# Performance work log

Hardware: AMD Instinct MI355X
Metric: run time of the kernel (lower is better)

The kernel has to match this reference:

```python
import jax, jax.numpy as jnp
import numpy as np
import itertools

X_SAMPLES = 2
N_POINTS = 96
NUM_REPS = 4
DIMS = (1, 3, 5, 7)   # SO(3)-style rep dims 2l+1
MAX_DIM = 7
NUM_CG = 4            # CG multiplicity index 'g'
NUM_CH = 16
NUM_LAYERS = 3
L_INPUT = 3           # input rep index; DIMS[3] = 7 matches X's dim


def _cplx_contractor(n):
    # T[a1..an, k]: re/im components of i^(a1+...+an); contracting n (re,im)
    # pairs against T yields their complex product. Matches cplx_lib.cplx_contractor.
    comps = [(1.0, 0.0), (0.0, 1.0), (-1.0, 0.0), (0.0, -1.0)]
    T = np.zeros((2,) * (n + 1), dtype=np.float32)
    for idx in itertools.product((0, 1), repeat=n):
        re, im = comps[sum(idx) % 4]
        T[idx + (0,)] = re
        T[idx + (1,)] = im
    return T


def _make_cg(rng):
    # CG-like buffer with selection-rule sparsity: entries outside each rep's
    # true dimension are zero, and (l, m -> q) only couples when |l-m|<=q<=l+m.
    cg = rng.standard_normal((NUM_CG, NUM_REPS, MAX_DIM, NUM_REPS, MAX_DIM,
                              NUM_REPS, MAX_DIM, 2)).astype(np.float32)
    mask = np.zeros_like(cg)
    for l in range(NUM_REPS):
        for m in range(NUM_REPS):
            for q in range(NUM_REPS):
                if abs(l - m) <= q <= l + m:
                    mask[:, l, :DIMS[l], m, :DIMS[m], q, :DIMS[q], :] = 1.0
    return cg * mask


def setup_inputs() -> dict:
    key = jax.random.key(0)
    k1, k2, k3, k4 = jax.random.split(key, 4)
    X = jax.random.normal(k1, (X_SAMPLES, N_POINTS, DIMS[L_INPUT], 2), jnp.float32)
    V = jax.random.normal(k2, (X_SAMPLES, N_POINTS, NUM_REPS, NUM_CH, MAX_DIM, 2), jnp.float32)
    # per-layer parameters, init scales matching the torch module
    f = jax.random.normal(k3, (NUM_LAYERS, NUM_REPS, NUM_CG, 2), jnp.float32) / (NUM_REPS + 1) ** 2
    W = jax.random.normal(k4, (NUM_LAYERS, NUM_REPS, NUM_CH, NUM_CG, NUM_CH, 2), jnp.float32) / (NUM_CH + 1) ** 2
    cg = jnp.asarray(_make_cg(np.random.default_rng(0)))
    C4 = jnp.asarray(_cplx_contractor(4))
    return {"X": X, "l": L_INPUT, "V": V, "cg": cg, "f": f, "W": W, "C4": C4}


def reference(X, l, V, cg, f, W, C4):
    # dX[x,i,j] = X[x,j] - X[x,i]  (torch: -(X[:,:,None] - X[:,None,:]))
    dX = X[:, None, :, :, :] - X[:, :, None, :, :]
    x, n = X.shape[0], X.shape[1]
    num_reps, max_dim = cg.shape[1], cg.shape[2]
    dim_l = X.shape[-2]
    # filters: (x, n, n, num_reps, max_dim, 2) with dX embedded at rep l
    base = jnp.zeros((x, n, n, num_reps, max_dim, 2), X.dtype)
    base = base.at[:, :, :, l, :dim_l, :].set(dX)
    for k in range(f.shape[0]):
        # equivariant quadratic nonlinearity on the pairwise filters
        filt = base + jnp.einsum(
            'glsmtqrv,xijlsw,xijmty,qgz,vwyzk->xijqrk',
            cg, base, base, f[k], C4, optimize='optimal')
        # CG tensor-product of filters with features, mixing channels via W
        V = jnp.einsum(
            'glsmtqrv,xijlsw,xjmctu,qcgdy,vwuyz->xiqdrz',
            cg, filt, V, W[k], C4, optimize='optimal')
    return V
```

## Files before the change

### kernel.cpp

```cpp
#include <hip/hip_runtime.h>
#include <hip/hip_bf16.h>

#define XS   2
#define NP   96
#define NLAY 3
#define NXI  (XS*NP)
#define VBF_ARR (XS*256*96)

__constant__ int P2R_c[16] = {0, 1,1,1, 2,2,2,2,2, 3,3,3,3,3,3,3};
__constant__ int P2D_c[16] = {0, 0,1,2, 0,1,2,3,4, 0,1,2,3,4,5,6};
__constant__ int DIMS_c[4] = {1,3,5,7};
__constant__ int OFF_c[4]  = {0,1,4,9};

typedef __attribute__((ext_vector_type(8))) short bf16x8;
typedef __attribute__((ext_vector_type(4))) float f32x4;

__device__ inline float2 cmadd(float2 acc, float2 a, float2 b){
    acc.x += a.x*b.x - a.y*b.y;
    acc.y += a.x*b.y + a.y*b.x;
    return acc;
}
__device__ inline unsigned short f2bf(float v){
    __hip_bfloat16 h = __float2bfloat16(v);
    union { __hip_bfloat16 h; unsigned short u; } cv; cv.h = h; return cv.u;
}
__device__ inline float bf2f(unsigned short u){
    union { unsigned short u; __hip_bfloat16 h; } cv; cv.u = u;
    return __bfloat162float(cv.h);
}

__global__ __launch_bounds__(256)
void prep_filt_kernel(const float* __restrict__ cg,
                      const float* __restrict__ f,
                      const float* __restrict__ Vin,
                      const float* __restrict__ X,
                      unsigned short* __restrict__ PKbf,
                      unsigned short* __restrict__ Vbf0,
                      float* __restrict__ filt_g)
{
    __shared__ float2 cgf_s[784];
    __shared__ float2 dX_s[NP][7];

    const int tid = threadIdx.x;
    if (blockIdx.x < 256){
        int idx = blockIdx.x*256 + tid;
        if (idx < 16384){
            int id = idx;
            int lm = id & 255;
            int qg = id >> 8;
            int ls = lm >> 4, mt = lm & 15;
            int qr = qg >> 2, g = qg & 3;
            int l = P2R_c[ls], s = P2D_c[ls];
            int m = P2R_c[mt], t = P2D_c[mt];
            int q = P2R_c[qr], r = P2D_c[qr];
            size_t co = (((((((size_t)g*4 + l)*7 + s)*4 + m)*7 + t)*4 + q)*7 + r);
            float re = cg[co*2], im = cg[co*2+1];
            unsigned short rh = f2bf(re), rl = f2bf(re - bf2f(rh));
            unsigned short ih = f2bf(im), il = f2bf(im - bf2f(ih));
            PKbf[0*16384 + id] = rh;
            PKbf[1*16384 + id] = rl;
            PKbf[2*16384 + id] = ih;
            PKbf[3*16384 + id] = il;
            PKbf[4*16384 + id] = ih ^ 0x8000;
            PKbf[5*16384 + id] = il ^ 0x8000;
        } else {
            int id = idx - 16384;
            int kj = id % 96;
            int n  = (id / 96) % 256;
            int x  = id / (96*256);
            int mt = n >> 4, c = n & 15;
            int m = P2R_c[mt], t = P2D_c[mt];
            const float* p = Vin + ((((size_t)(x*NP + kj)*4 + m)*16 + c)*7 + t)*2;
            float re = p[0], im = p[1];
            unsigned short h;
            h = f2bf(re); Vbf0[0*VBF_ARR + id] = h;
            Vbf0[1*VBF_ARR + id] = f2bf(re - bf2f(h));
            h = f2bf(im); Vbf0[2*VBF_ARR + id] = h;
            Vbf0[3*VBF_ARR + id] = f2bf(im - bf2f(h));
        }
        return;
    }

    const int fb = blockIdx.x - 256;
    const int k  = fb / NXI;
    const int xi = fb % NXI;
    const int x = xi / NP, i = xi % NP;

    for (int u = tid; u < 784; u += 256){
        int qr = u / 49, st = u % 49;
        int s = st / 7, t = st % 7;
        int q = P2R_c[qr], r = P2D_c[qr];
        float2 acc = make_float2(0.f, 0.f);
        #pragma unroll
        for (int g = 0; g < 4; ++g){
            const float* cgp = cg + (((((((size_t)g*4+3)*7 + s)*4 + 3)*7 + t)*4 + q)*7 + r)*2;
            const float* fp  = f + ((k*4 + q)*4 + g)*2;
            acc = cmadd(acc, make_float2(cgp[0], cgp[1]), make_float2(fp[0], fp[1]));
        }
        cgf_s[u] = acc;
    }
    for (int e = tid; e < NP*7; e += 256){
        int j = e / 7, s = e % 7;
        const float* Xj = X + (((size_t)x*NP + j)*7 + s)*2;
        const float* Xi = X + (((size_t)x*NP + i)*7 + s)*2;
        dX_s[j][s] = make_float2(Xj[0]-Xi[0], Xj[1]-Xi[1]);
    }
    __syncthreads();

    float2* out = (float2*)filt_g + (size_t)fb*NP*16;
    for (int e = tid; e < NP*16; e += 256){
        int j = e >> 4, qr = e & 15;
        const float2* cb = cgf_s + qr*49;
        float2 acc = make_float2(0.f, 0.f);
        #pragma unroll
        for (int s = 0; s < 7; ++s){
            float2 inner = make_float2(0.f, 0.f);
            #pragma unroll
            for (int t = 0; t < 7; ++t)
                inner = cmadd(inner, cb[s*7 + t], dX_s[j][t]);
            acc = cmadd(acc, dX_s[j][s], inner);
        }
        if (qr >= 9){ float2 dv = dX_s[j][qr-9]; acc.x += dv.x; acc.y += dv.y; }
        out[e] = acc;
    }
}

template<int LAST>
__global__ __launch_bounds__(512, 2)
void TS_kernel(const float* __restrict__ filt_gk,
               const unsigned short* __restrict__ PKbf,
               const float* __restrict__ W_k,
               const unsigned short* __restrict__ Vbf_in,
               unsigned short* __restrict__ Vbf_out,
               float* __restrict__ Dout)
{
    __shared__ __align__(16) unsigned short Abuf[6][16][104];
    __shared__ __align__(16) unsigned short T2buf[4][16][264];
    float2* S_s = (float2*)&Abuf[0][0][0];

    const int tid = threadIdx.x;
    const int xi = blockIdx.x;
    const int x = xi / NP, i = xi % NP;

    for (int e = tid; e < NP*16; e += 512){
        const int j = e >> 4, ls = e & 15;
        float2 fv = ((const float2*)filt_gk)[((size_t)xi*NP + j)*16 + ls];
        unsigned short h = f2bf(fv.x);
        Abuf[0][ls][j] = h;
        Abuf[1][ls][j] = f2bf(fv.x - bf2f(h));
        h = f2bf(fv.y);
        unsigned short lo = f2bf(fv.y - bf2f(h));
        Abuf[2][ls][j] = h;
        Abuf[3][ls][j] = lo;
        Abuf[4][ls][j] = h  ^ 0x8000;
        Abuf[5][ls][j] = lo ^ 0x8000;
    }
    __syncthreads();

    const int w    = tid >> 6;
    const int lane = tid & 63;
    const int lrow = lane & 15;
    const int kb   = (lane >> 4) * 8;

    {
        f32x4 accR[2], accI[2];
        #pragma unroll
        for (int nt = 0; nt < 2; ++nt){
            accR[nt] = (f32x4){0.f,0.f,0.f,0.f};
            accI[nt] = (f32x4){0.f,0.f,0.f,0.f};
        }
        const unsigned short* Vrh = Vbf_in + 0*VBF_ARR + (size_t)x*256*96;
        const unsigned short* Vrl = Vbf_in + 1*VBF_ARR + (size_t)x*256*96;
        const unsigned short* Vih = Vbf_in + 2*VBF_ARR + (size_t)x*256*96;
        const unsigned short* Vil = Vbf_in + 3*VBF_ARR + (size_t)x*256*96;
        #pragma unroll
        for (int kt = 0; kt < 3; ++kt){
            const int ka = kt*32 + kb;
            bf16x8 frh = *(const bf16x8*)&Abuf[0][lrow][ka];
            bf16x8 frl = *(const bf16x8*)&Abuf[1][lrow][ka];
            bf16x8 fih = *(const bf16x8*)&Abuf[2][lrow][ka];
            bf16x8 fil = *(const bf16x8*)&Abuf[3][lrow][ka];
            bf16x8 nfh = *(const bf16x8*)&Abuf[4][lrow][ka];
            bf16x8 nfl = *(const bf16x8*)&Abuf[5][lrow][ka];
            #pragma unroll
            for (int nt = 0; nt < 2; ++nt){
                const int n = w*32 + nt*16 + lrow;
                const size_t bo = (size_t)n*96 + ka;
                bf16x8 vrh = *(const bf16x8*)(Vrh + bo);
                bf16x8 vrl = *(const bf16x8*)(Vrl + bo);
                bf16x8 vih = *(const bf16x8*)(Vih + bo);
                bf16x8 vil = *(const bf16x8*)(Vil + bo);
                accR[nt] = __builtin_amdgcn_mfma_f32_16x16x32_bf16(frh, vrh, accR[nt], 0,0,0);
                accR[nt] = __builtin_amdgcn_mfma_f32_16x16x32_bf16(frh, vrl, accR[nt], 0,0,0);
                accR[nt] = __builtin_amdgcn_mfma_f32_16x16x32_bf16(frl, vrh, accR[nt], 0,0,0);
                accR[nt] = __builtin_amdgcn_mfma_f32_16x16x32_bf16(nfh, vih, accR[nt], 0,0,0);
                accR[nt] = __builtin_amdgcn_mfma_f32_16x16x32_bf16(nfh, vil, accR[nt], 0,0,0);
                accR[nt] = __builtin_amdgcn_mfma_f32_16x16x32_bf16(nfl, vih, accR[nt], 0,0,0);
                accI[nt] = __builtin_amdgcn_mfma_f32_16x16x32_bf16(frh, vih, accI[nt], 0,0,0);
                accI[nt] = __builtin_amdgcn_mfma_f32_16x16x32_bf16(frh, vil, accI[nt], 0,0,0);
                accI[nt] = __builtin_amdgcn_mfma_f32_16x16x32_bf16(frl, vih, accI[nt], 0,0,0);
                accI[nt] = __builtin_amdgcn_mfma_f32_16x16x32_bf16(fih, vrh, accI[nt], 0,0,0);
                accI[nt] = __builtin_amdgcn_mfma_f32_16x16x32_bf16(fih, vrl, accI[nt], 0,0,0);
                accI[nt] = __builtin_amdgcn_mfma_f32_16x16x32_bf16(fil, vrh, accI[nt], 0,0,0);
            }
        }
        #pragma unroll
        for (int nt = 0; nt < 2; ++nt){
            #pragma unroll
            for (int r = 0; r < 4; ++r){
                const int lmp = ((lane>>4)*4 + r)*16 + (w*2 + nt);
                float tr = accR[nt][r], ti = accI[nt][r];
                unsigned short h = f2bf(tr);
                T2buf[0][lrow][lmp] = h;
                T2buf[1][lrow][lmp] = f2bf(tr - bf2f(h));
                h = f2bf(ti);
                T2buf[2][lrow][lmp] = h;
                T2buf[3][lrow][lmp] = f2bf(ti - bf2f(h));
            }
        }
    }
    __syncthreads();

    {
        const int qtile = w & 3;
        const int kh    = w >> 2;
        f32x4 sR = (f32x4){0.f,0.f,0.f,0.f};
        f32x4 sI = (f32x4){0.f,0.f,0.f,0.f};
        #pragma unroll
        for (int kt4 = 0; kt4 < 4; ++kt4){
            const int kt = kh*4 + kt4;
            const int ka = kt*32 + kb;
            const size_t arow = (size_t)(qtile*16 + lrow)*256 + ka;
            bf16x8 prh = *(const bf16x8*)(PKbf + 0*16384 + arow);
            bf16x8 prl = *(const bf16x8*)(PKbf + 1*16384 + arow);
            bf16x8 pih = *(const bf16x8*)(PKbf + 2*16384 + arow);
            bf16x8 pil = *(const bf16x8*)(PKbf + 3*16384 + arow);
            bf16x8 pnh = *(const bf16x8*)(PKbf + 4*16384 + arow);
            bf16x8 pnl = *(const bf16x8*)(PKbf + 5*16384 + arow);
            bf16x8 trh = *(const bf16x8*)&T2buf[0][lrow][ka];
            bf16x8 trl = *(const bf16x8*)&T2buf[1][lrow][ka];
            bf16x8 tih = *(const bf16x8*)&T2buf[2][lrow][ka];
            bf16x8 til = *(const bf16x8*)&T2buf[3][lrow][ka];
            sR = __builtin_amdgcn_mfma_f32_16x16x32_bf16(prh, trh, sR, 0,0,0);
            sR = __builtin_amdgcn_mfma_f32_16x16x32_bf16(prh, trl, sR, 0,0,0);
            sR = __builtin_amdgcn_mfma_f32_16x16x32_bf16(prl, trh, sR, 0,0,0);
            sR = __builtin_amdgcn_mfma_f32_16x16x32_bf16(pnh, tih, sR, 0,0,0);
            sR = __builtin_amdgcn_mfma_f32_16x16x32_bf16(pnh, til, sR, 0,0,0);
            sR = __builtin_amdgcn_mfma_f32_16x16x32_bf16(pnl, tih, sR, 0,0,0);
            sI = __builtin_amdgcn_mfma_f32_16x16x32_bf16(prh, tih, sI, 0,0,0);
            sI = __builtin_amdgcn_mfma_f32_16x16x32_bf16(prh, til, sI, 0,0,0);
            sI = __builtin_amdgcn_mfma_f32_16x16x32_bf16(prl, tih, sI, 0,0,0);
            sI = __builtin_amdgcn_mfma_f32_16x16x32_bf16(pih, trh, sI, 0,0,0);
            sI = __builtin_amdgcn_mfma_f32_16x16x32_bf16(pih, trl, sI, 0,0,0);
            sI = __builtin_amdgcn_mfma_f32_16x16x32_bf16(pil, trh, sI, 0,0,0);
        }
        if (kh == 0){
            #pragma unroll
            for (int r = 0; r < 4; ++r)
                S_s[((size_t)qtile*16 + (lane>>4)*4 + r)*16 + lrow] =
                    make_float2(sR[r], sI[r]);
        }
        __syncthreads();
        if (kh == 1){
            #pragma unroll
            for (int r = 0; r < 4; ++r){
                const size_t si = ((size_t)qtile*16 + (lane>>4)*4 + r)*16 + lrow;
                float2 sp = S_s[si];
                sp.x += sR[r]; sp.y += sI[r];
                S_s[si] = sp;
            }
        }
        __syncthreads();
    }

    if (tid < 256){
        const int qr2 = tid >> 4, d = tid & 15;
        const int q = P2R_c[qr2];
        float2 acc = make_float2(0.f, 0.f);
        const float2* Wb = (const float2*)W_k + (size_t)q*16*4*16 + d;
        #pragma unroll 4
        for (int c = 0; c < 16; ++c){
            #pragma unroll
            for (int g = 0; g < 4; ++g){
                acc = cmadd(acc, S_s[((size_t)qr2*4 + g)*16 + c], Wb[(c*4 + g)*16]);
            }
        }
        if (LAST){
            const int r = P2D_c[qr2];
            ((float2*)Dout)[((size_t)xi*4 + q)*112 + d*7 + r] = acc;
        } else {
            const size_t vo = ((size_t)x*256 + tid)*96 + i;
            unsigned short h;
            h = f2bf(acc.x); Vbf_out[0*VBF_ARR + vo] = h;
            Vbf_out[1*VBF_ARR + vo] = f2bf(acc.x - bf2f(h));
            h = f2bf(acc.y); Vbf_out[2*VBF_ARR + vo] = h;
            Vbf_out[3*VBF_ARR + vo] = f2bf(acc.y - bf2f(h));
        }
    } else if (LAST){
        const int u = tid - 256;
        if (u < 192){
            int q, base, span;
            if (u < 96)      { q = 0; base = 0;   span = 6; }
            else if (u < 160){ q = 1; base = 96;  span = 4; }
            else             { q = 2; base = 160; span = 2; }
            const int v = u - base;
            const int d = v / span;
            const int r = DIMS_c[q] + v % span;
            ((float2*)Dout)[((size_t)xi*4 + q)*112 + d*7 + r] = make_float2(0.f, 0.f);
        }
    }
}

extern "C" void kernel_launch(void* const* d_in, const int* in_sizes, int n_in,
                              void* d_out, int out_size, void* d_ws, size_t ws_size,
                              hipStream_t stream) {
    const float* X  = (const float*)d_in[0];
    const float* V  = (const float*)d_in[2];
    const float* cg = (const float*)d_in[3];
    const float* f  = (const float*)d_in[4];
    const float* W  = (const float*)d_in[5];

    float* ws    = (float*)d_ws;
    unsigned short* PKbf = (unsigned short*)ws;
    unsigned short* VbfA = (unsigned short*)(ws + 49152);
    unsigned short* VbfB = (unsigned short*)(ws + 49152 + 98304);
    float* filt_g = ws + 49152 + 98304 + 98304;

    prep_filt_kernel<<<256 + NLAY*NXI, 256, 0, stream>>>(cg, f, V, X, PKbf, VbfA, filt_g);

    const float* W0 = W;
    const float* W1 = W + (size_t)1*4*16*4*16*2;
    const float* W2 = W + (size_t)2*4*16*4*16*2;
    const float* f0 = filt_g;
    const float* f1 = filt_g + (size_t)1*NXI*NP*16*2;
    const float* f2 = filt_g + (size_t)2*NXI*NP*16*2;

    TS_kernel<0><<<NXI, 512, 0, stream>>>(f0, PKbf, W0, VbfA, VbfB, nullptr);
    TS_kernel<0><<<NXI, 512, 0, stream>>>(f1, PKbf, W1, VbfB, VbfA, nullptr);
    TS_kernel<1><<<NXI, 512, 0, stream>>>(f2, PKbf, W2, VbfA, VbfB, (float*)d_out);
}
```

Baseline: 69.27 us.

## Fuse prep and three layer kernels into one cooperative kernel with grid syncs

Replaces the four separate launches (prep/filter plus three tensor-product layers) with a single cooperative kernel of 192 blocks that uses grid-wide syncs between layers. Each block now computes its own per-layer filter directly into shared memory as split bf16, instead of writing fp32 filters to global memory and reading them back. This removes launch gaps and the global filter round trip. In exchange it adds grid barrier costs, runs the initial packing on fewer threads, and depends on all blocks being co-resident.

```diff
diff --git a/kernel.cpp b/kernel.cpp
--- a/kernel.cpp
+++ b/kernel.cpp
@@ -1,5 +1,6 @@
 #include <hip/hip_runtime.h>
 #include <hip/hip_bf16.h>
+#include <hip/hip_cooperative_groups.h>
 
 #define XS   2
 #define NP   96
@@ -7,6 +8,8 @@
 #define NXI  (XS*NP)
 #define VBF_ARR (XS*256*96)
 
+namespace cgx = cooperative_groups;
+
 __constant__ int P2R_c[16] = {0, 1,1,1, 2,2,2,2,2, 3,3,3,3,3,3,3};
 __constant__ int P2D_c[16] = {0, 0,1,2, 0,1,2,3,4, 0,1,2,3,4,5,6};
 __constant__ int DIMS_c[4] = {1,3,5,7};
@@ -29,23 +32,33 @@
     return __bfloat162float(cv.h);
 }
 
-__global__ __launch_bounds__(256)
-void prep_filt_kernel(const float* __restrict__ cg,
-                      const float* __restrict__ f,
-                      const float* __restrict__ Vin,
-                      const float* __restrict__ X,
-                      unsigned short* __restrict__ PKbf,
-                      unsigned short* __restrict__ Vbf0,
-                      float* __restrict__ filt_g)
+__global__ __launch_bounds__(512)
+void fused_kernel(const float* __restrict__ cg,
+                  const float* __restrict__ f,
+                  const float* __restrict__ Vin,
+                  const float* __restrict__ X,
+                  const float* __restrict__ W,
+                  unsigned short* __restrict__ PKbf,
+                  unsigned short* __restrict__ VbfA,
+                  unsigned short* __restrict__ VbfB,
+                  float* __restrict__ Dout)
 {
+    __shared__ float2 dX_s[NP][7];
     __shared__ float2 cgf_s[784];
-    __shared__ float2 dX_s[NP][7];
+    __shared__ __align__(16) unsigned short Abuf[6][16][104];
+    __shared__ __align__(16) unsigned short T2buf[4][16][264];
+    float2* S_s = (float2*)&Abuf[0][0][0];
+
+    cgx::grid_group grid = cgx::this_grid();
 
     const int tid = threadIdx.x;
-    if (blockIdx.x < 256){
-        int idx = blockIdx.x*256 + tid;
-        if (idx < 16384){
-            int id = idx;
+    const int xi = blockIdx.x;
+    const int x = xi / NP, i = xi % NP;
+
+    {
+        const int gidx = xi*512 + tid;
+        if (gidx < 16384){
+            int id = gidx;
             int lm = id & 255;
             int qg = id >> 8;
             int ls = lm >> 4, mt = lm & 15;
@@ -63,250 +76,232 @@
             PKbf[3*16384 + id] = il;
             PKbf[4*16384 + id] = ih ^ 0x8000;
             PKbf[5*16384 + id] = il ^ 0x8000;
-        } else {
-            int id = idx - 16384;
+        } else if (gidx < 65536){
+            int id = gidx - 16384;
             int kj = id % 96;
             int n  = (id / 96) % 256;
-            int x  = id / (96*256);
+            int xx = id / (96*256);
             int mt = n >> 4, c = n & 15;
             int m = P2R_c[mt], t = P2D_c[mt];
-            const float* p = Vin + ((((size_t)(x*NP + kj)*4 + m)*16 + c)*7 + t)*2;
+            const float* p = Vin + ((((size_t)(xx*NP + kj)*4 + m)*16 + c)*7 + t)*2;
             float re = p[0], im = p[1];
             unsigned short h;
-            h = f2bf(re); Vbf0[0*VBF_ARR + id] = h;
-            Vbf0[1*VBF_ARR + id] = f2bf(re - bf2f(h));
-            h = f2bf(im); Vbf0[2*VBF_ARR + id] = h;
-            Vbf0[3*VBF_ARR + id] = f2bf(im - bf2f(h));
-        }
-        return;
+            h = f2bf(re); VbfA[0*VBF_ARR + id] = h;
+            VbfA[1*VBF_ARR + id] = f2bf(re - bf2f(h));
+            h = f2bf(im); VbfA[2*VBF_ARR + id] = h;
+            VbfA[3*VBF_ARR + id] = f2bf(im - bf2f(h));
+        }
     }
-
-    const int fb = blockIdx.x - 256;
-    const int k  = fb / NXI;
-    const int xi = fb % NXI;
-    const int x = xi / NP, i = xi % NP;
-
-    for (int u = tid; u < 784; u += 256){
-        int qr = u / 49, st = u % 49;
-        int s = st / 7, t = st % 7;
-        int q = P2R_c[qr], r = P2D_c[qr];
-        float2 acc = make_float2(0.f, 0.f);
-        #pragma unroll
-        for (int g = 0; g < 4; ++g){
-            const float* cgp = cg + (((((((size_t)g*4+3)*7 + s)*4 + 3)*7 + t)*4 + q)*7 + r)*2;
-            const float* fp  = f + ((k*4 + q)*4 + g)*2;
-            acc = cmadd(acc, make_float2(cgp[0], cgp[1]), make_float2(fp[0], fp[1]));
-        }
-        cgf_s[u] = acc;
-    }
-    for (int e = tid; e < NP*7; e += 256){
+    for (int e = tid; e < NP*7; e += 512){
         int j = e / 7, s = e % 7;
         const float* Xj = X + (((size_t)x*NP + j)*7 + s)*2;
         const float* Xi = X + (((size_t)x*NP + i)*7 + s)*2;
         dX_s[j][s] = make_float2(Xj[0]-Xi[0], Xj[1]-Xi[1]);
     }
-    __syncthreads();
-
-    float2* out = (float2*)filt_g + (size_t)fb*NP*16;
-    for (int e = tid; e < NP*16; e += 256){
-        int j = e >> 4, qr = e & 15;
-        const float2* cb = cgf_s + qr*49;
-        float2 acc = make_float2(0.f, 0.f);
-        #pragma unroll
-        for (int s = 0; s < 7; ++s){
-            float2 inner = make_float2(0.f, 0.f);
-            #pragma unroll
-            for (int t = 0; t < 7; ++t)
-                inner = cmadd(inner, cb[s*7 + t], dX_s[j][t]);
-            acc = cmadd(acc, dX_s[j][s], inner);
-        }
-        if (qr >= 9){ float2 dv = dX_s[j][qr-9]; acc.x += dv.x; acc.y += dv.y; }
-        out[e] = acc;
-    }
-}
-
-template<int LAST>
-__global__ __launch_bounds__(512, 2)
-void TS_kernel(const float* __restrict__ filt_gk,
-               const unsigned short* __restrict__ PKbf,
-               const float* __restrict__ W_k,
-               const unsigned short* __restrict__ Vbf_in,
-               unsigned short* __restrict__ Vbf_out,
-               float* __restrict__ Dout)
-{
-    __shared__ __align__(16) unsigned short Abuf[6][16][104];
-    __shared__ __align__(16) unsigned short T2buf[4][16][264];
-    float2* S_s = (float2*)&Abuf[0][0][0];
-
-    const int tid = threadIdx.x;
-    const int xi = blockIdx.x;
-    const int x = xi / NP, i = xi % NP;
-
-    for (int e = tid; e < NP*16; e += 512){
-        const int j = e >> 4, ls = e & 15;
-        float2 fv = ((const float2*)filt_gk)[((size_t)xi*NP + j)*16 + ls];
-        unsigned short h = f2bf(fv.x);
-        Abuf[0][ls][j] = h;
-        Abuf[1][ls][j] = f2bf(fv.x - bf2f(h));
-        h = f2bf(fv.y);
-        unsigned short lo = f2bf(fv.y - bf2f(h));
-        Abuf[2][ls][j] = h;
-        Abuf[3][ls][j] = lo;
-        Abuf[4][ls][j] = h  ^ 0x8000;
-        Abuf[5][ls][j] = lo ^ 0x8000;
-    }
-    __syncthreads();
+    __threadfence();
+    grid.sync();
 
     const int w    = tid >> 6;
     const int lane = tid & 63;
     const int lrow = lane & 15;
     const int kb   = (lane >> 4) * 8;
 
-    {
-        f32x4 accR[2], accI[2];
-        #pragma unroll
-        for (int nt = 0; nt < 2; ++nt){
-            accR[nt] = (f32x4){0.f,0.f,0.f,0.f};
-            accI[nt] = (f32x4){0.f,0.f,0.f,0.f};
-        }
-        const unsigned short* Vrh = Vbf_in + 0*VBF_ARR + (size_t)x*256*96;
-        const unsigned short* Vrl = Vbf_in + 1*VBF_ARR + (size_t)x*256*96;
-        const unsigned short* Vih = Vbf_in + 2*VBF_ARR + (size_t)x*256*96;
-        const unsigned short* Vil = Vbf_in + 3*VBF_ARR + (size_t)x*256*96;
-        #pragma unroll
-        for (int kt = 0; kt < 3; ++kt){
-            const int ka = kt*32 + kb;
-            bf16x8 frh = *(const bf16x8*)&Abuf[0][lrow][ka];
-            bf16x8 frl = *(const bf16x8*)&Abuf[1][lrow][ka];
-            bf16x8 fih = *(const bf16x8*)&Abuf[2][lrow][ka];
-            bf16x8 fil = *(const bf16x8*)&Abuf[3][lrow][ka];
-            bf16x8 nfh = *(const bf16x8*)&Abuf[4][lrow][ka];
-            bf16x8 nfl = *(const bf16x8*)&Abuf[5][lrow][ka];
+    for (int k = 0; k < NLAY; ++k){
+        const unsigned short* Vbf_in  = (k & 1) ? VbfB : VbfA;
+        unsigned short*       Vbf_out = (k & 1) ? VbfA : VbfB;
+        const float* W_k = W + (size_t)k*4*16*4*16*2;
+
+        for (int u = tid; u < 784; u += 512){
+            int qr = u / 49, st = u % 49;
+            int s = st / 7, t = st % 7;
+            int q = P2R_c[qr], r = P2D_c[qr];
+            float2 acc = make_float2(0.f, 0.f);
+            #pragma unroll
+            for (int g = 0; g < 4; ++g){
+                const float* cgp = cg + (((((((size_t)g*4+3)*7 + s)*4 + 3)*7 + t)*4 + q)*7 + r)*2;
+                const float* fp  = f + ((k*4 + q)*4 + g)*2;
+                acc = cmadd(acc, make_float2(cgp[0], cgp[1]), make_float2(fp[0], fp[1]));
+            }
+            cgf_s[u] = acc;
+        }
+        __syncthreads();
+
+        for (int e = tid; e < NP*16; e += 512){
+            int j = e >> 4, qr = e & 15;
+            const float2* cb = cgf_s + qr*49;
+            float2 acc = make_float2(0.f, 0.f);
+            #pragma unroll
+            for (int s = 0; s < 7; ++s){
+                float2 inner = make_float2(0.f, 0.f);
+                #pragma unroll
+                for (int t = 0; t < 7; ++t)
+                    inner = cmadd(inner, cb[s*7 + t], dX_s[j][t]);
+                acc = cmadd(acc, dX_s[j][s], inner);
+            }
+            if (qr >= 9){ float2 dv = dX_s[j][qr-9]; acc.x += dv.x; acc.y += dv.y; }
+            unsigned short h = f2bf(acc.x);
+            Abuf[0][qr][j] = h;
+            Abuf[1][qr][j] = f2bf(acc.x - bf2f(h));
+            h = f2bf(acc.y);
+            unsigned short lo = f2bf(acc.y - bf2f(h));
+            Abuf[2][qr][j] = h;
+            Abuf[3][qr][j] = lo;
+            Abuf[4][qr][j] = h  ^ 0x8000;
+            Abuf[5][qr][j] = lo ^ 0x8000;
+        }
+        __syncthreads();
+
+        {
+            f32x4 accR[2], accI[2];
             #pragma unroll
             for (int nt = 0; nt < 2; ++nt){
-                const int n = w*32 + nt*16 + lrow;
-                const size_t bo = (size_t)n*96 + ka;
-                bf16x8 vrh = *(const bf16x8*)(Vrh + bo);
-                bf16x8 vrl = *(const bf16x8*)(Vrl + bo);
-                bf16x8 vih = *(const bf16x8*)(Vih + bo);
-                bf16x8 vil = *(const bf16x8*)(Vil + bo);
-                accR[nt] = __builtin_amdgcn_mfma_f32_16x16x32_bf16(frh, vrh, accR[nt], 0,0,0);
-                accR[nt] = __builtin_amdgcn_mfma_f32_16x16x32_bf16(frh, vrl, accR[nt], 0,0,0);
-                accR[nt] = __builtin_amdgcn_mfma_f32_16x16x32_bf16(frl, vrh, accR[nt], 0,0,0);
-                accR[nt] = __builtin_amdgcn_mfma_f32_16x16x32_bf16(nfh, vih, accR[nt], 0,0,0);
-                accR[nt] = __builtin_amdgcn_mfma_f32_16x16x32_bf16(nfh, vil, accR[nt], 0,0,0);
-                accR[nt] = __builtin_amdgcn_mfma_f32_16x16x32_bf16(nfl, vih, accR[nt], 0,0,0);
-                accI[nt] = __builtin_amdgcn_mfma_f32_16x16x32_bf16(frh, vih, accI[nt], 0,0,0);
-                accI[nt] = __builtin_amdgcn_mfma_f32_16x16x32_bf16(frh, vil, accI[nt], 0,0,0);
-                accI[nt] = __builtin_amdgcn_mfma_f32_16x16x32_bf16(frl, vih, accI[nt], 0,0,0);
-                accI[nt] = __builtin_amdgcn_mfma_f32_16x16x32_bf16(fih, vrh, accI[nt], 0,0,0);
-                accI[nt] = __builtin_amdgcn_mfma_f32_16x16x32_bf16(fih, vrl, accI[nt], 0,0,0);
-                accI[nt] = __builtin_amdgcn_mfma_f32_16x16x32_bf16(fil, vrh, accI[nt], 0,0,0);
-            }
-        }
-        #pragma unroll
-        for (int nt = 0; nt < 2; ++nt){
-            #pragma unroll
-            for (int r = 0; r < 4; ++r){
-                const int lmp = ((lane>>4)*4 + r)*16 + (w*2 + nt);
-                float tr = accR[nt][r], ti = accI[nt][r];
-                unsigned short h = f2bf(tr);
-                T2buf[0][lrow][lmp] = h;
-                T2buf[1][lrow][lmp] = f2bf(tr - bf2f(h));
-                h = f2bf(ti);
-                T2buf[2][lrow][lmp] = h;
-                T2buf[3][lrow][lmp] = f2bf(ti - bf2f(h));
-            }
-        }
-    }
-    __syncthreads();
-
-    {
-        const int qtile = w & 3;
-        const int kh    = w >> 2;
-        f32x4 sR = (f32x4){0.f,0.f,0.f,0.f};
-        f32x4 sI = (f32x4){0.f,0.f,0.f,0.f};
-        #pragma unroll
-        for (int kt4 = 0; kt4 < 4; ++kt4){
-            const int kt = kh*4 + kt4;
-            const int ka = kt*32 + kb;
-            const size_t arow = (size_t)(qtile*16 + lrow)*256 + ka;
-            bf16x8 prh = *(const bf16x8*)(PKbf + 0*16384 + arow);
-            bf16x8 prl = *(const bf16x8*)(PKbf + 1*16384 + arow);
-            bf16x8 pih = *(const bf16x8*)(PKbf + 2*16384 + arow);
-            bf16x8 pil = *(const bf16x8*)(PKbf + 3*16384 + arow);
-            bf16x8 pnh = *(const bf16x8*)(PKbf + 4*16384 + arow);
-            bf16x8 pnl = *(const bf16x8*)(PKbf + 5*16384 + arow);
-            bf16x8 trh = *(const bf16x8*)&T2buf[0][lrow][ka];
-            bf16x8 trl = *(const bf16x8*)&T2buf[1][lrow][ka];
-            bf16x8 tih = *(const bf16x8*)&T2buf[2][lrow][ka];
-            bf16x8 til = *(const bf16x8*)&T2buf[3][lrow][ka];
-            sR = __builtin_amdgcn_mfma_f32_16x16x32_bf16(prh, trh, sR, 0,0,0);
-            sR = __builtin_amdgcn_mfma_f32_16x16x32_bf16(prh, trl, sR, 0,0,0);
-            sR = __builtin_amdgcn_mfma_f32_16x16x32_bf16(prl, trh, sR, 0,0,0);
-            sR = __builtin_amdgcn_mfma_f32_16x16x32_bf16(pnh, tih, sR, 0,0,0);
-            sR = __builtin_amdgcn_mfma_f32_16x16x32_bf16(pnh, til, sR, 0,0,0);
-            sR = __builtin_amdgcn_mfma_f32_16x16x32_bf16(pnl, tih, sR, 0,0,0);
-            sI = __builtin_amdgcn_mfma_f32_16x16x32_bf16(prh, tih, sI, 0,0,0);
-            sI = __builtin_amdgcn_mfma_f32_16x16x32_bf16(prh, til, sI, 0,0,0);
-            sI = __builtin_amdgcn_mfma_f32_16x16x32_bf16(prl, tih, sI, 0,0,0);
-            sI = __builtin_amdgcn_mfma_f32_16x16x32_bf16(pih, trh, sI, 0,0,0);
-            sI = __builtin_amdgcn_mfma_f32_16x16x32_bf16(pih, trl, sI, 0,0,0);
-            sI = __builtin_amdgcn_mfma_f32_16x16x32_bf16(pil, trh, sI, 0,0,0);
-        }
-        if (kh == 0){
-            #pragma unroll
-            for (int r = 0; r < 4; ++r)
-                S_s[((size_t)qtile*16 + (lane>>4)*4 + r)*16 + lrow] =
-                    make_float2(sR[r], sI[r]);
+                accR[nt] = (f32x4){0.f,0.f,0.f,0.f};
+                accI[nt] = (f32x4){0.f,0.f,0.f,0.f};
+            }
+            const unsigned short* Vrh = Vbf_in + 0*VBF_ARR + (size_t)x*256*96;
+            const unsigned short* Vrl = Vbf_in + 1*VBF_ARR + (size_t)x*256*96;
+            const unsigned short* Vih = Vbf_in + 2*VBF_ARR + (size_t)x*256*96;
+            const unsigned short* Vil = Vbf_in + 3*VBF_ARR + (size_t)x*256*96;
+            #pragma unroll
+            for (int kt = 0; kt < 3; ++kt){
+                const int ka = kt*32 + kb;
+                bf16x8 frh = *(const bf16x8*)&Abuf[0][lrow][ka];
+                bf16x8 frl = *(const bf16x8*)&Abuf[1][lrow][ka];
+                bf16x8 fih = *(const bf16x8*)&Abuf[2][lrow][ka];
+                bf16x8 fil = *(const bf16x8*)&Abuf[3][lrow][ka];
+                bf16x8 nfh = *(const bf16x8*)&Abuf[4][lrow][ka];
+                bf16x8 nfl = *(const bf16x8*)&Abuf[5][lrow][ka];
+                #pragma unroll
+                for (int nt = 0; nt < 2; ++nt){
+                    const int n = w*32 + nt*16 + lrow;
+                    const size_t bo = (size_t)n*96 + ka;
+                    bf16x8 vrh = *(const bf16x8*)(Vrh + bo);
+                    bf16x8 vrl = *(const bf16x8*)(Vrl + bo);
+                    bf16x8 vih = *(const bf16x8*)(Vih + bo);
+                    bf16x8 vil = *(const bf16x8*)(Vil + bo);
+                    accR[nt] = __builtin_amdgcn_mfma_f32_16x16x32_bf16(frh, vrh, accR[nt], 0,0,0);
+                    accR[nt] = __builtin_amdgcn_mfma_f32_16x16x32_bf16(frh, vrl, accR[nt], 0,0,0);
+                    accR[nt] = __builtin_amdgcn_mfma_f32_16x16x32_bf16(frl, vrh, accR[nt], 0,0,0);
+                    accR[nt] = __builtin_amdgcn_mfma_f32_16x16x32_bf16(nfh, vih, accR[nt], 0,0,0);
+                    accR[nt] = __builtin_amdgcn_mfma_f32_16x16x32_bf16(nfh, vil, accR[nt], 0,0,0);
+                    accR[nt] = __builtin_amdgcn_mfma_f32_16x16x32_bf16(nfl, vih, accR[nt], 0,0,0);
+                    accI[nt] = __builtin_amdgcn_mfma_f32_16x16x32_bf16(frh, vih, accI[nt], 0,0,0);
+                    accI[nt] = __builtin_amdgcn_mfma_f32_16x16x32_bf16(frh, vil, accI[nt], 0,0,0);
+                    accI[nt] = __builtin_amdgcn_mfma_f32_16x16x32_bf16(frl, vih, accI[nt], 0,0,0);
+                    accI[nt] = __builtin_amdgcn_mfma_f32_16x16x32_bf16(fih, vrh, accI[nt], 0,0,0);
+                    accI[nt] = __builtin_amdgcn_mfma_f32_16x16x32_bf16(fih, vrl, accI[nt], 0,0,0);
+                    accI[nt] = __builtin_amdgcn_mfma_f32_16x16x32_bf16(fil, vrh, accI[nt], 0,0,0);
+                }
+            }
+            #pragma unroll
+            for (int nt = 0; nt < 2; ++nt){
+                #pragma unroll
+                for (int r = 0; r < 4; ++r){
+                    const int lmp = ((lane>>4)*4 + r)*16 + (w*2 + nt);
+                    float tr = accR[nt][r], ti = accI[nt][r];
+                    unsigned short h = f2bf(tr);
+                    T2buf[0][lrow][lmp] = h;
+                    T2buf[1][lrow][lmp] = f2bf(tr - bf2f(h));
+                    h = f2bf(ti);
+                    T2buf[2][lrow][lmp] = h;
+                    T2buf[3][lrow][lmp] = f2bf(ti - bf2f(h));
+                }
+            }
         }
         __syncthreads();
-        if (kh == 1){
-            #pragma unroll
-            for (int r = 0; r < 4; ++r){
-                const size_t si = ((size_t)qtile*16 + (lane>>4)*4 + r)*16 + lrow;
-                float2 sp = S_s[si];
-                sp.x += sR[r]; sp.y += sI[r];
-                S_s[si] = sp;
-            }
-        }
-        __syncthreads();
-    }
-
-    if (tid < 256){
-        const int qr2 = tid >> 4, d = tid & 15;
-        const int q = P2R_c[qr2];
-        float2 acc = make_float2(0.f, 0.f);
-        const float2* Wb = (const float2*)W_k + (size_t)q*16*4*16 + d;
-        #pragma unroll 4
-        for (int c = 0; c < 16; ++c){
-            #pragma unroll
-            for (int g = 0; g < 4; ++g){
-                acc = cmadd(acc, S_s[((size_t)qr2*4 + g)*16 + c], Wb[(c*4 + g)*16]);
-            }
-        }
-        if (LAST){
-            const int r = P2D_c[qr2];
-            ((float2*)Dout)[((size_t)xi*4 + q)*112 + d*7 + r] = acc;
-        } else {
-            const size_t vo = ((size_t)x*256 + tid)*96 + i;
-            unsigned short h;
-            h = f2bf(acc.x); Vbf_out[0*VBF_ARR + vo] = h;
-            Vbf_out[1*VBF_ARR + vo] = f2bf(acc.x - bf2f(h));
-            h = f2bf(acc.y); Vbf_out[2*VBF_ARR + vo] = h;
-            Vbf_out[3*VBF_ARR + vo] = f2bf(acc.y - bf2f(h));
-        }
-    } else if (LAST){
-        const int u = tid - 256;
-        if (u < 192){
-            int q, base, span;
-            if (u < 96)      { q = 0; base = 0;   span = 6; }
-            else if (u < 160){ q = 1; base = 96;  span = 4; }
-            else             { q = 2; base = 160; span = 2; }
-            const int v = u - base;
-            const int d = v / span;
-            const int r = DIMS_c[q] + v % span;
-            ((float2*)Dout)[((size_t)xi*4 + q)*112 + d*7 + r] = make_float2(0.f, 0.f);
+
+        {
+            const int qtile = w & 3;
+            const int kh    = w >> 2;
+            f32x4 sR = (f32x4){0.f,0.f,0.f,0.f};
+            f32x4 sI = (f32x4){0.f,0.f,0.f,0.f};
+            #pragma unroll
+            for (int kt4 = 0; kt4 < 4; ++kt4){
+                const int kt = kh*4 + kt4;
+                const int ka = kt*32 + kb;
+                const size_t arow = (size_t)(qtile*16 + lrow)*256 + ka;
+                bf16x8 prh = *(const bf16x8*)(PKbf + 0*16384 + arow);
+                bf16x8 prl = *(const bf16x8*)(PKbf + 1*16384 + arow);
+                bf16x8 pih = *(const bf16x8*)(PKbf + 2*16384 + arow);
+                bf16x8 pil = *(const bf16x8*)(PKbf + 3*16384 + arow);
+                bf16x8 pnh = *(const bf16x8*)(PKbf + 4*16384 + arow);
+                bf16x8 pnl = *(const bf16x8*)(PKbf + 5*16384 + arow);
+                bf16x8 trh = *(const bf16x8*)&T2buf[0][lrow][ka];
+                bf16x8 trl = *(const bf16x8*)&T2buf[1][lrow][ka];
+                bf16x8 tih = *(const bf16x8*)&T2buf[2][lrow][ka];
+                bf16x8 til = *(const bf16x8*)&T2buf[3][lrow][ka];
+                sR = __builtin_amdgcn_mfma_f32_16x16x32_bf16(prh, trh, sR, 0,0,0);
+                sR = __builtin_amdgcn_mfma_f32_16x16x32_bf16(prh, trl, sR, 0,0,0);
+                sR = __builtin_amdgcn_mfma_f32_16x16x32_bf16(prl, trh, sR, 0,0,0);
+                sR = __builtin_amdgcn_mfma_f32_16x16x32_bf16(pnh, tih, sR, 0,0,0);
+                sR = __builtin_amdgcn_mfma_f32_16x16x32_bf16(pnh, til, sR, 0,0,0);
+                sR = __builtin_amdgcn_mfma_f32_16x16x32_bf16(pnl, tih, sR, 0,0,0);
+                sI = __builtin_amdgcn_mfma_f32_16x16x32_bf16(prh, tih, sI, 0,0,0);
+                sI = __builtin_amdgcn_mfma_f32_16x16x32_bf16(prh, til, sI, 0,0,0);
+                sI = __builtin_amdgcn_mfma_f32_16x16x32_bf16(prl, tih, sI, 0,0,0);
+                sI = __builtin_amdgcn_mfma_f32_16x16x32_bf16(pih, trh, sI, 0,0,0);
+                sI = __builtin_amdgcn_mfma_f32_16x16x32_bf16(pih, trl, sI, 0,0,0);
+                sI = __builtin_amdgcn_mfma_f32_16x16x32_bf16(pil, trh, sI, 0,0,0);
+            }
+            if (kh == 0){
+                #pragma unroll
+                for (int r = 0; r < 4; ++r)
+                    S_s[((size_t)qtile*16 + (lane>>4)*4 + r)*16 + lrow] =
+                        make_float2(sR[r], sI[r]);
+            }
+            __syncthreads();
+            if (kh == 1){
+                #pragma unroll
+                for (int r = 0; r < 4; ++r){
+                    const size_t si = ((size_t)qtile*16 + (lane>>4)*4 + r)*16 + lrow;
+                    float2 sp = S_s[si];
+                    sp.x += sR[r]; sp.y += sI[r];
+                    S_s[si] = sp;
+                }
+            }
+            __syncthreads();
+        }
+
+        if (tid < 256){
+            const int qr2 = tid >> 4, d = tid & 15;
+            const int q = P2R_c[qr2];
+            float2 acc = make_float2(0.f, 0.f);
+            const float2* Wb = (const float2*)W_k + (size_t)q*16*4*16 + d;
+            #pragma unroll 4
+            for (int c = 0; c < 16; ++c){
+                #pragma unroll
+                for (int g = 0; g < 4; ++g){
+                    acc = cmadd(acc, S_s[((size_t)qr2*4 + g)*16 + c], Wb[(c*4 + g)*16]);
+                }
+            }
+            if (k == NLAY-1){
+                const int r = P2D_c[qr2];
+                ((float2*)Dout)[((size_t)xi*4 + q)*112 + d*7 + r] = acc;
+            } else {
+                const size_t vo = ((size_t)x*256 + tid)*96 + i;
+                unsigned short h;
+                h = f2bf(acc.x); Vbf_out[0*VBF_ARR + vo] = h;
+                Vbf_out[1*VBF_ARR + vo] = f2bf(acc.x - bf2f(h));
+                h = f2bf(acc.y); Vbf_out[2*VBF_ARR + vo] = h;
+                Vbf_out[3*VBF_ARR + vo] = f2bf(acc.y - bf2f(h));
+            }
+        } else if (k == NLAY-1){
+            const int u = tid - 256;
+            if (u < 192){
+                int q, base, span;
+                if (u < 96)      { q = 0; base = 0;   span = 6; }
+                else if (u < 160){ q = 1; base = 96;  span = 4; }
+                else             { q = 2; base = 160; span = 2; }
+                const int v = u - base;
+                const int d = v / span;
+                const int r = DIMS_c[q] + v % span;
+                ((float2*)Dout)[((size_t)xi*4 + q)*112 + d*7 + r] = make_float2(0.f, 0.f);
+            }
+        }
+
+        if (k < NLAY-1){
+            __threadfence();
+            grid.sync();
         }
     }
 }
@@ -324,18 +319,12 @@
     unsigned short* PKbf = (unsigned short*)ws;
     unsigned short* VbfA = (unsigned short*)(ws + 49152);
     unsigned short* VbfB = (unsigned short*)(ws + 49152 + 98304);
-    float* filt_g = ws + 49152 + 98304 + 98304;
-
-    prep_filt_kernel<<<256 + NLAY*NXI, 256, 0, stream>>>(cg, f, V, X, PKbf, VbfA, filt_g);
-
-    const float* W0 = W;
-    const float* W1 = W + (size_t)1*4*16*4*16*2;
-    const float* W2 = W + (size_t)2*4*16*4*16*2;
-    const float* f0 = filt_g;
-    const float* f1 = filt_g + (size_t)1*NXI*NP*16*2;
-    const float* f2 = filt_g + (size_t)2*NXI*NP*16*2;
-
-    TS_kernel<0><<<NXI, 512, 0, stream>>>(f0, PKbf, W0, VbfA, VbfB, nullptr);
-    TS_kernel<0><<<NXI, 512, 0, stream>>>(f1, PKbf, W1, VbfB, VbfA, nullptr);
-    TS_kernel<1><<<NXI, 512, 0, stream>>>(f2, PKbf, W2, VbfA, VbfB, (float*)d_out);
-}
+    float* Dout = (float*)d_out;
+
+    void* args[] = {
+        (void*)&cg, (void*)&f, (void*)&V, (void*)&X, (void*)&W,
+        (void*)&PKbf, (void*)&VbfA, (void*)&VbfB, (void*)&Dout
+    };
+    hipLaunchCooperativeKernel((const void*)fused_kernel,
+                               dim3(NXI), dim3(512), args, 0, stream);
+}
```

New measurement: 258.3 us. 273% more time.
